# Kernel tuning notes

Hardware: AMD Instinct MI355X
Metric: run time of the kernel (lower is better)

## Reference

```python
import jax, jax.numpy as jnp
import numpy as np
from jax import lax

DG = 16          # deformable_groups
K = 9            # 3x3 kernel taps
PAD = 1
MAX_RES = 10.0   # max_residue_magnitude


def conv3x3(x, w, b):
    # NCHW / OIHW, stride 1, SAME padding (pad=1 for 3x3)
    return lax.conv_general_dilated(x, w, (1, 1), 'SAME',
                                    dimension_numbers=('NCHW', 'OIHW', 'NCHW')) + b[None, :, None, None]


def lrelu(x):
    return jnp.where(x >= 0, x, 0.1 * x)


def setup_inputs() -> dict:
    key = jax.random.key(0)
    ks = jax.random.split(key, 10)
    B, C, H, W = 4, 64, 128, 128
    Cout = 64
    coff_in = 2 * C + 2          # (1 + pa_frames//2)*C + pa_frames, pa_frames=2
    nch = 3 * K * DG             # 432 offset/mask channels

    def mkw(k, o, i, scale=1.0):
        return jax.random.normal(k, (o, i, 3, 3), jnp.float32) * (scale / np.sqrt(i * 9))

    return {
        'x': jax.random.normal(ks[0], (B, C, H, W), jnp.float32),
        'x_flow_warped': jax.random.normal(ks[1], (B, C, H, W), jnp.float32),
        'x_current': jax.random.normal(ks[2], (B, C, H, W), jnp.float32),
        'flow': jax.random.normal(ks[3], (B, 2, H, W), jnp.float32) * 2.0,
        'w1': mkw(ks[4], Cout, coff_in), 'b1': jnp.zeros((Cout,), jnp.float32),
        'w2': mkw(ks[5], Cout, Cout),    'b2': jnp.zeros((Cout,), jnp.float32),
        'w3': mkw(ks[6], Cout, Cout),    'b3': jnp.zeros((Cout,), jnp.float32),
        'w4': mkw(ks[7], nch, Cout, 0.1), 'b4': jnp.zeros((nch,), jnp.float32),
        'weight': mkw(ks[8], Cout, C),   'bias': jnp.zeros((Cout,), jnp.float32),
    }


def deform_conv2d(x, offset, mask, weight, bias):
    # modulated deformable conv, 3x3, stride 1, pad 1, dilation 1, groups=1
    B, C, H, W = x.shape
    O = weight.shape[0]
    dg, Cg = DG, C // DG
    off = offset.reshape(B, dg, K, 2, H, W)
    dy, dx = off[:, :, :, 0], off[:, :, :, 1]        # (B,dg,K,H,W), (y,x) pairs
    ki = jnp.arange(3)
    ii, jj = jnp.meshgrid(ki, ki, indexing='ij')
    ii = ii.reshape(K).astype(jnp.float32)
    jj = jj.reshape(K).astype(jnp.float32)
    # sampling coords in input space: h - pad + i + dy, w - pad + j + dx
    py = dy + (jnp.arange(H, dtype=jnp.float32) - PAD)[None, None, None, :, None] + ii[None, None, :, None, None]
    px = dx + (jnp.arange(W, dtype=jnp.float32) - PAD)[None, None, None, None, :] + jj[None, None, :, None, None]
    y0 = jnp.floor(py)
    x0 = jnp.floor(px)
    wy1 = py - y0
    wx1 = px - x0
    y0i = y0.astype(jnp.int32)
    x0i = x0.astype(jnp.int32)
    xg = x.reshape(B, dg, Cg, H * W)

    def gather(yi, xi):
        valid = ((yi >= 0) & (yi < H) & (xi >= 0) & (xi < W)).astype(x.dtype)  # zero outside
        idx = (jnp.clip(yi, 0, H - 1) * W + jnp.clip(xi, 0, W - 1)).reshape(B, dg, 1, K * H * W)
        v = jnp.take_along_axis(xg, jnp.broadcast_to(idx, (B, dg, Cg, K * H * W)), axis=-1)
        return v.reshape(B, dg, Cg, K, H, W) * valid[:, :, None]

    s = (gather(y0i, x0i)         * ((1 - wy1) * (1 - wx1))[:, :, None]
         + gather(y0i, x0i + 1)   * ((1 - wy1) * wx1)[:, :, None]
         + gather(y0i + 1, x0i)   * (wy1 * (1 - wx1))[:, :, None]
         + gather(y0i + 1, x0i + 1) * (wy1 * wx1)[:, :, None])
    s = s * mask.reshape(B, dg, 1, K, H, W)
    s = s.reshape(B, C, K, H, W)
    return jnp.einsum('bckhw,ock->bohw', s, weight.reshape(O, C, K)) + bias[None, :, None, None]


def reference(x, x_flow_warped, x_current, flow, w1, b1, w2, b2, w3, b3, w4, b4, weight, bias):
    feat = jnp.concatenate([x_flow_warped, x_current, flow], axis=1)
    h = lrelu(conv3x3(feat, w1, b1))
    h = lrelu(conv3x3(h, w2, b2))
    h = lrelu(conv3x3(h, w3, b3))
    out = conv3x3(h, w4, b4)
    o1, o2, mask = jnp.split(out, 3, axis=1)
    offset = MAX_RES * jnp.tanh(jnp.concatenate([o1, o2], axis=1))
    flowf = flow[:, ::-1]  # flip (x,y) -> (y,x)
    offset = offset + jnp.tile(flowf, (1, offset.shape[1] // 2, 1, 1))
    mask = jax.nn.sigmoid(mask)
    return deform_conv2d(x, offset, mask, weight, bias)
```

## Files before the change

### kernel.cpp

```cpp
#include <hip/hip_runtime.h>
#include <math.h>
#include <type_traits>

#define BH 4
#define HH 128
#define WW 128
#define HW (HH * WW)
#define SSTR 600

typedef __attribute__((ext_vector_type(8))) short bf16x8;
typedef __attribute__((ext_vector_type(4))) float f32x4;

__device__ inline short f2bf(float f) {
    union { float f; unsigned u; } x; x.f = f;
    unsigned r = x.u + 0x7fff + ((x.u >> 16) & 1);
    return (short)(r >> 16);
}
__device__ inline float bf2f(short h) {
    union { unsigned u; float f; } x; x.u = ((unsigned)(unsigned short)h) << 16;
    return x.f;
}
__device__ inline float bflo(unsigned u) {
    union { unsigned u; float f; } x; x.u = u << 16; return x.f;
}
__device__ inline float bfhi(unsigned u) {
    union { unsigned u; float f; } x; x.u = u & 0xffff0000u; return x.f;
}

struct RepackArgs {
    const float* w[5];
    short* dst[5];
    int off[6];
};

__device__ inline void repack_generic(const float* w, short* dst, int g,
                                      int M, int Cin, int T, int MT)
{
    int lane = g & 63;
    int f = g >> 6;
    int mt = f % MT;
    int kt = f / MT;
    int tap = kt % T;
    int kc = kt / T;
    int m = mt * 16 + (lane & 15);
    int ic0 = kc * 32 + (lane >> 4) * 8;
    short v[8];
#pragma unroll
    for (int i = 0; i < 8; ++i) {
        int ic = ic0 + i;
        float x = (m < M && ic < Cin) ? w[((size_t)m * Cin + ic) * T + tap] : 0.f;
        v[i] = f2bf(x);
    }
    *(bf16x8*)(dst + (size_t)g * 8) = *(const bf16x8*)v;
}

__global__ __launch_bounds__(256) void repack_all_k(RepackArgs a)
{
    int g = blockIdx.x * 256 + threadIdx.x;
    if (g < a.off[1]) {
        repack_generic(a.w[0], a.dst[0], g - a.off[0], 64, 130, 9, 4);
    } else if (g < a.off[2]) {
        repack_generic(a.w[1], a.dst[1], g - a.off[1], 64, 64, 9, 4);
    } else if (g < a.off[3]) {
        repack_generic(a.w[2], a.dst[2], g - a.off[2], 64, 64, 9, 4);
    } else if (g < a.off[4]) {
        repack_generic(a.w[3], a.dst[3], g - a.off[3], 432, 64, 9, 27);
    } else if (g < a.off[5]) {
        int gg = g - a.off[4];
        int lane = gg & 63;
        int f = gg >> 6;
        int mt = f & 3, kc = f >> 2;
        int m = mt * 16 + (lane & 15);
        int ck0 = kc * 32 + (lane >> 4) * 8;
        short v[8];
#pragma unroll
        for (int i = 0; i < 8; ++i) {
            int ck = ck0 + i;
            int dg = ck / 36, rem = ck % 36;
            int k = rem >> 2, cg = rem & 3;
            int c = dg * 4 + cg;
            v[i] = f2bf(a.w[4][((size_t)m * 64 + c) * 9 + k]);
        }
        *(bf16x8*)(a.dst[4] + (size_t)gg * 8) = *(const bf16x8*)v;
    }
}

__global__ __launch_bounds__(256) void prep_k(
    const float* __restrict__ xfw, const float* __restrict__ xcur,
    const float* __restrict__ flow, const float* __restrict__ x,
    short* __restrict__ cc, short* __restrict__ xt)
{
    int tid = threadIdx.x;
    int z = blockIdx.z;
    int px = blockIdx.x * 256 + tid;
    if (z < BH) {
        int b = z;
        const float* s0 = xfw + (size_t)b * 64 * HW + px;
        const float* s1 = xcur + (size_t)b * 64 * HW + px;
        const float* s2 = flow + (size_t)b * 2 * HW + px;
        short v[144];
#pragma unroll
        for (int c = 0; c < 64; ++c) v[c] = f2bf(s0[(size_t)c * HW]);
#pragma unroll
        for (int c = 0; c < 64; ++c) v[64 + c] = f2bf(s1[(size_t)c * HW]);
        v[128] = f2bf(s2[0]);
        v[129] = f2bf(s2[HW]);
#pragma unroll
        for (int c = 130; c < 144; ++c) v[c] = 0;
        short* dst = cc + ((size_t)b * HW + px) * 144;
#pragma unroll
        for (int q = 0; q < 18; ++q)
            *(bf16x8*)(dst + q * 8) = *(const bf16x8*)&v[q * 8];
    } else {
        int b = z - BH;
        const float* src = x + (size_t)b * 64 * HW + px;
        short v[64];
#pragma unroll
        for (int c = 0; c < 64; ++c) v[c] = f2bf(src[(size_t)c * HW]);
        short* dstb = xt + (size_t)b * 16 * HW * 4 + (size_t)px * 4;
#pragma unroll
        for (int d = 0; d < 16; ++d)
            *(uint2*)(dstb + (size_t)d * HW * 4) = *(const uint2*)&v[d * 4];
    }
}

template<int CSTR, int KC, bool ACT, int MTW>
__global__ __launch_bounds__(256) void conv_mfma_k(
    const short* __restrict__ in, const short* __restrict__ wp,
    const float* __restrict__ bias, short* __restrict__ out,
    int Cout, int MB, int MT)
{
    __shared__ alignas(16) short X[3 * 66 * 40];
    const int tid = threadIdx.x;
    const int lane = tid & 63, wv = tid >> 6;
    const int x0 = blockIdx.x * 64, y = blockIdx.y;
    const int zb = blockIdx.z;
    const int b = zb / MB, mb = zb % MB;

    int mtg[MTW];
#pragma unroll
    for (int mt = 0; mt < MTW; ++mt) {
        int t = (mb * 4 + wv) * MTW + mt;
        mtg[mt] = (t < MT) ? t : MT - 1;
    }

    const int r = tid / 66, c = tid - r * 66;
    const int yy = y + r - 1, xx = x0 + c - 1;
    const bool inb = (tid < 198) && (yy >= 0 && yy < HH && xx >= 0 && xx < WW);
    const short* srcp = in + ((size_t)b * HW + (size_t)yy * WW + xx) * CSTR;
    short* dstp = &X[(r * 66 + c) * 40];

    f32x4 acc[MTW][4] = {};

    for (int kc = 0; kc < KC; ++kc) {
        __syncthreads();
        if (tid < 198) {
            if (inb) {
                const short* s0 = srcp + kc * 32;
#pragma unroll
                for (int g = 0; g < 4; ++g)
                    *(bf16x8*)&dstp[g * 8] = *(const bf16x8*)&s0[g * 8];
            } else {
                bf16x8 z = {};
#pragma unroll
                for (int g = 0; g < 4; ++g) *(bf16x8*)&dstp[g * 8] = z;
            }
        }
        __syncthreads();
#pragma unroll
        for (int tap = 0; tap < 9; ++tap) {
            const int dy = tap / 3, dx = tap - dy * 3;
            bf16x8 a[MTW];
#pragma unroll
            for (int mt = 0; mt < MTW; ++mt)
                a[mt] = *(const bf16x8*)(wp + (((size_t)(kc * 9 + tap) * MT + mtg[mt]) * 64 + lane) * 8);
#pragma unroll
            for (int nt = 0; nt < 4; ++nt) {
                int cc2 = nt * 16 + (lane & 15) + dx;
                bf16x8 bb = *(const bf16x8*)&X[(dy * 66 + cc2) * 40 + (lane >> 4) * 8];
#pragma unroll
                for (int mt = 0; mt < MTW; ++mt)
                    acc[mt][nt] = __builtin_amdgcn_mfma_f32_16x16x32_bf16(a[mt], bb, acc[mt][nt], 0, 0, 0);
            }
        }
    }

    const int xl = lane & 15, rg = lane >> 4;
#pragma unroll
    for (int mt = 0; mt < MTW; ++mt) {
        int t = (mb * 4 + wv) * MTW + mt;
        int m0 = t * 16;
        if (m0 >= Cout) continue;
#pragma unroll
        for (int nt = 0; nt < 4; ++nt) {
            int xx2 = x0 + nt * 16 + xl;
            short pk[4];
#pragma unroll
            for (int j = 0; j < 4; ++j) {
                int o = m0 + rg * 4 + j;
                float rv = acc[mt][nt][j] + bias[o];
                if (ACT) rv = (rv >= 0.f) ? rv : 0.1f * rv;
                pk[j] = f2bf(rv);
            }
            *(uint2*)(out + ((size_t)b * HW + (size_t)y * WW + xx2) * (size_t)Cout
                      + m0 + rg * 4) = *(const uint2*)pk;
        }
    }
}

__global__ __launch_bounds__(256) void dcn_k(
    const short* __restrict__ xt, const float* __restrict__ flow,
    const short* __restrict__ out4, const short* __restrict__ wtp,
    const float* __restrict__ bias, float* __restrict__ out)
{
    __shared__ alignas(16) short s[16 * SSTR];
    const int tid = threadIdx.x;
    const int b = blockIdx.z, y = blockIdx.y, xb = blockIdx.x * 16;
    const size_t hw = (size_t)HW;
    constexpr float L2E = 1.4426950408889634f;

    const int lane = tid & 63, wv = tid >> 6;
    const int p = tid & 15;
    const int dg = tid >> 4;
    const int xp = xb + p;
    const size_t pix = (size_t)y * WW + xp;
    const short* xg = xt + ((size_t)b * 16 + dg) * hw * 4;
    const short* o4p = out4 + ((size_t)b * hw + pix) * 432;
    const float fl0 = flow[((size_t)b * 2 + 0) * hw + pix];
    const float fl1 = flow[((size_t)b * 2 + 1) * hw + pix];

    const unsigned* pd = (const unsigned*)o4p + 9 * dg;
    const short* pm = o4p + 288 + 9 * dg;
    short* sp = &s[p * SSTR + dg * 36];

#pragma unroll
    for (int it = 0; it < 9; ++it) {
        unsigned dyx = pd[it];
        float omk = bf2f(pm[it]);
        float ody = bflo(dyx), odx = bfhi(dyx);
        float tdy = 1.f - 2.f * __builtin_amdgcn_rcpf(__builtin_amdgcn_exp2f(2.f * L2E * ody) + 1.f);
        float tdx = 1.f - 2.f * __builtin_amdgcn_rcpf(__builtin_amdgcn_exp2f(2.f * L2E * odx) + 1.f);
        float m   = __builtin_amdgcn_rcpf(1.f + __builtin_amdgcn_exp2f(-L2E * omk));

        float py = 10.f * tdy + fl1 + (float)(y  - 1 + it / 3);
        float px = 10.f * tdx + fl0 + (float)(xp - 1 + it % 3);
        float fy = floorf(py), fx = floorf(px);
        int iy0 = (int)fy, ix0 = (int)fx;
        float wy1 = py - fy, wx1 = px - fx;
        float wy0 = 1.f - wy1, wx0 = 1.f - wx1;
        int iy1 = iy0 + 1, ix1 = ix0 + 1;
        bool vy0 = (iy0 >= 0) & (iy0 < HH), vy1 = (iy1 >= 0) & (iy1 < HH);
        bool vx0 = (ix0 >= 0) & (ix0 < WW), vx1 = (ix1 >= 0) & (ix1 < WW);
        float w00 = (vy0 & vx0) ? wy0 * wx0 : 0.f;
        float w01 = (vy0 & vx1) ? wy0 * wx1 : 0.f;
        float w10 = (vy1 & vx0) ? wy1 * wx0 : 0.f;
        float w11 = (vy1 & vx1) ? wy1 * wx1 : 0.f;
        int cy0 = min(max(iy0, 0), HH - 1), cy1 = min(max(iy1, 0), HH - 1);
        int cx0 = min(max(ix0, 0), WW - 1), cx1 = min(max(ix1, 0), WW - 1);
        uint2 d00 = *(const uint2*)(xg + (size_t)(cy0 * WW + cx0) * 4);
        uint2 d01 = *(const uint2*)(xg + (size_t)(cy0 * WW + cx1) * 4);
        uint2 d10 = *(const uint2*)(xg + (size_t)(cy1 * WW + cx0) * 4);
        uint2 d11 = *(const uint2*)(xg + (size_t)(cy1 * WW + cx1) * 4);

        float a0 = w00 * bflo(d00.x) + w01 * bflo(d01.x) + w10 * bflo(d10.x) + w11 * bflo(d11.x);
        float a1 = w00 * bfhi(d00.x) + w01 * bfhi(d01.x) + w10 * bfhi(d10.x) + w11 * bfhi(d11.x);
        float a2 = w00 * bflo(d00.y) + w01 * bflo(d01.y) + w10 * bflo(d10.y) + w11 * bflo(d11.y);
        float a3 = w00 * bfhi(d00.y) + w01 * bfhi(d01.y) + w10 * bfhi(d10.y) + w11 * bfhi(d11.y);

        uint2 t;
        t.x = ((unsigned)(unsigned short)f2bf(a1 * m) << 16) | (unsigned short)f2bf(a0 * m);
        t.y = ((unsigned)(unsigned short)f2bf(a3 * m) << 16) | (unsigned short)f2bf(a2 * m);
        *(uint2*)&sp[it * 4] = t;
    }
    __syncthreads();

    f32x4 acc = {};
#pragma unroll
    for (int kc = 0; kc < 18; ++kc) {
        bf16x8 a = *(const bf16x8*)(wtp + ((size_t)(kc * 4 + wv) * 64 + lane) * 8);
        bf16x8 bb = *(const bf16x8*)&s[(lane & 15) * SSTR + kc * 32 + (lane >> 4) * 8];
        acc = __builtin_amdgcn_mfma_f32_16x16x32_bf16(a, bb, acc, 0, 0, 0);
    }

    const int xl = lane & 15, rg = lane >> 4;
#pragma unroll
    for (int j = 0; j < 4; ++j) {
        int o = wv * 16 + rg * 4 + j;
        out[((size_t)(b * 64 + o) * HH + y) * WW + xb + xl] = acc[j] + bias[o];
    }
}

extern "C" void kernel_launch(void* const* d_in, const int* in_sizes, int n_in,
                              void* d_out, int out_size, void* d_ws, size_t ws_size,
                              hipStream_t stream)
{
    const float* x    = (const float*)d_in[0];
    const float* xfw  = (const float*)d_in[1];
    const float* xcur = (const float*)d_in[2];
    const float* flow = (const float*)d_in[3];
    const float* w1   = (const float*)d_in[4];
    const float* b1   = (const float*)d_in[5];
    const float* w2   = (const float*)d_in[6];
    const float* b2   = (const float*)d_in[7];
    const float* w3   = (const float*)d_in[8];
    const float* b3   = (const float*)d_in[9];
    const float* w4   = (const float*)d_in[10];
    const float* b4   = (const float*)d_in[11];
    const float* wt   = (const float*)d_in[12];
    const float* bs   = (const float*)d_in[13];

    const size_t hw = (size_t)HW;
    short* out4 = (short*)d_ws;
    short* h1   = out4 + (size_t)BH * hw * 432;
    short* h2   = h1 + (size_t)BH * hw * 64;
    short* cc   = h2 + (size_t)BH * hw * 64;
    short* xt   = cc + (size_t)BH * hw * 144 + 256;
    short* wp1  = xt + (size_t)BH * hw * 64 + 256;
    short* wp2  = wp1 + (size_t)180 * 512;
    short* wp3  = wp2 + (size_t)72 * 512;
    short* wp4  = wp3 + (size_t)72 * 512;
    short* wtp  = wp4 + (size_t)486 * 512;

    RepackArgs ra;
    ra.w[0] = w1; ra.w[1] = w2; ra.w[2] = w3; ra.w[3] = w4; ra.w[4] = wt;
    ra.dst[0] = wp1; ra.dst[1] = wp2; ra.dst[2] = wp3; ra.dst[3] = wp4; ra.dst[4] = wtp;
    int tot[5] = {11520, 4608, 4608, 31104, 4608};
    ra.off[0] = 0;
    for (int i = 0; i < 5; ++i) ra.off[i + 1] = ra.off[i] + tot[i];
    repack_all_k<<<(ra.off[5] + 255) / 256, 256, 0, stream>>>(ra);

    prep_k<<<dim3(HW / 256, 1, 2 * BH), 256, 0, stream>>>(xfw, xcur, flow, x, cc, xt);

    dim3 blk(256);
    conv_mfma_k<144, 5, true,  1><<<dim3(2, 128, BH),      blk, 0, stream>>>(cc, wp1, b1, h1, 64, 1, 4);
    conv_mfma_k<64,  2, true,  1><<<dim3(2, 128, BH),      blk, 0, stream>>>(h1, wp2, b2, h2, 64, 1, 4);
    conv_mfma_k<64,  2, true,  1><<<dim3(2, 128, BH),      blk, 0, stream>>>(h2, wp3, b3, h1, 64, 1, 4);
    conv_mfma_k<64,  2, false, 4><<<dim3(2, 128, BH * 2),  blk, 0, stream>>>(h1, wp4, b4, out4, 432, 2, 27);

    dcn_k<<<dim3(WW / 16, HH, BH), blk, 0, stream>>>(xt, flow, out4, wtp, bs, (float*)d_out);
}
```

Baseline: 205.3 us.

## Fuse tanh/sigmoid/flow offset epilogue into conv4 and register-prefetch conv input chunks

Moves the tanh, scale-by-10, flow addition and sigmoid mask activation from the deformable conv kernel into the epilogue of the last offset conv, so out4 now stores final offsets and masks and dcn_k drops its flow loads and transcendental work. Separately, the conv kernel now loads the next input channel chunk into registers while the MFMA loop runs on the current chunk, overlapping global loads with compute. Storing final offsets in bf16 instead of pre-activation values changes rounding: an offset of magnitude around 100 keeps less fractional precision, which can affect bilinear sampling accuracy.

New measurement: 236.8 us. 1.15x slower.

```diff
diff --git a/kernel.cpp b/kernel.cpp
--- a/kernel.cpp
+++ b/kernel.cpp
@@ -124,11 +124,11 @@
     }
 }
 
-template<int CSTR, int KC, bool ACT, int MTW>
+template<int CSTR, int KC, bool ACT, int MTW, bool DCNT>
 __global__ __launch_bounds__(256) void conv_mfma_k(
     const short* __restrict__ in, const short* __restrict__ wp,
-    const float* __restrict__ bias, short* __restrict__ out,
-    int Cout, int MB, int MT)
+    const float* __restrict__ bias, const float* __restrict__ flow,
+    short* __restrict__ out, int Cout, int MB, int MT)
 {
     __shared__ alignas(16) short X[3 * 66 * 40];
     const int tid = threadIdx.x;
@@ -136,6 +136,7 @@
     const int x0 = blockIdx.x * 64, y = blockIdx.y;
     const int zb = blockIdx.z;
     const int b = zb / MB, mb = zb % MB;
+    constexpr float L2E = 1.4426950408889634f;
 
     int mtg[MTW];
 #pragma unroll
@@ -146,27 +147,37 @@
 
     const int r = tid / 66, c = tid - r * 66;
     const int yy = y + r - 1, xx = x0 + c - 1;
-    const bool inb = (tid < 198) && (yy >= 0 && yy < HH && xx >= 0 && xx < WW);
+    const bool stg_act = (tid < 198);
+    const bool inb = stg_act && (yy >= 0 && yy < HH && xx >= 0 && xx < WW);
     const short* srcp = in + ((size_t)b * HW + (size_t)yy * WW + xx) * CSTR;
     short* dstp = &X[(r * 66 + c) * 40];
 
+    bf16x8 stg0 = {}, stg1 = {}, stg2 = {}, stg3 = {};
+    if (inb) {
+        stg0 = *(const bf16x8*)&srcp[0];
+        stg1 = *(const bf16x8*)&srcp[8];
+        stg2 = *(const bf16x8*)&srcp[16];
+        stg3 = *(const bf16x8*)&srcp[24];
+    }
+
     f32x4 acc[MTW][4] = {};
 
     for (int kc = 0; kc < KC; ++kc) {
         __syncthreads();
-        if (tid < 198) {
-            if (inb) {
-                const short* s0 = srcp + kc * 32;
-#pragma unroll
-                for (int g = 0; g < 4; ++g)
-                    *(bf16x8*)&dstp[g * 8] = *(const bf16x8*)&s0[g * 8];
-            } else {
-                bf16x8 z = {};
-#pragma unroll
-                for (int g = 0; g < 4; ++g) *(bf16x8*)&dstp[g * 8] = z;
-            }
+        if (stg_act) {
+            *(bf16x8*)&dstp[0]  = stg0;
+            *(bf16x8*)&dstp[8]  = stg1;
+            *(bf16x8*)&dstp[16] = stg2;
+            *(bf16x8*)&dstp[24] = stg3;
         }
         __syncthreads();
+        if (inb && kc + 1 < KC) {
+            const short* s0 = srcp + (kc + 1) * 32;
+            stg0 = *(const bf16x8*)&s0[0];
+            stg1 = *(const bf16x8*)&s0[8];
+            stg2 = *(const bf16x8*)&s0[16];
+            stg3 = *(const bf16x8*)&s0[24];
+        }
 #pragma unroll
         for (int tap = 0; tap < 9; ++tap) {
             const int dy = tap / 3, dx = tap - dy * 3;
@@ -187,19 +198,34 @@
 
     const int xl = lane & 15, rg = lane >> 4;
 #pragma unroll
-    for (int mt = 0; mt < MTW; ++mt) {
-        int t = (mb * 4 + wv) * MTW + mt;
-        int m0 = t * 16;
-        if (m0 >= Cout) continue;
-#pragma unroll
-        for (int nt = 0; nt < 4; ++nt) {
-            int xx2 = x0 + nt * 16 + xl;
+    for (int nt = 0; nt < 4; ++nt) {
+        int xx2 = x0 + nt * 16 + xl;
+        float fl0 = 0.f, fl1 = 0.f;
+        if (DCNT) {
+            size_t pix = (size_t)y * WW + xx2;
+            fl0 = flow[((size_t)b * 2 + 0) * HW + pix];
+            fl1 = flow[((size_t)b * 2 + 1) * HW + pix];
+        }
+#pragma unroll
+        for (int mt = 0; mt < MTW; ++mt) {
+            int t = (mb * 4 + wv) * MTW + mt;
+            int m0 = t * 16;
+            if (m0 >= Cout) continue;
             short pk[4];
 #pragma unroll
             for (int j = 0; j < 4; ++j) {
                 int o = m0 + rg * 4 + j;
                 float rv = acc[mt][nt][j] + bias[o];
                 if (ACT) rv = (rv >= 0.f) ? rv : 0.1f * rv;
+                if (DCNT) {
+                    if (o < 288) {
+                        float th = 1.f - 2.f * __builtin_amdgcn_rcpf(
+                            __builtin_amdgcn_exp2f(2.f * L2E * rv) + 1.f);
+                        rv = 10.f * th + ((o & 1) ? fl0 : fl1);
+                    } else {
+                        rv = __builtin_amdgcn_rcpf(1.f + __builtin_amdgcn_exp2f(-L2E * rv));
+                    }
+                }
                 pk[j] = f2bf(rv);
             }
             *(uint2*)(out + ((size_t)b * HW + (size_t)y * WW + xx2) * (size_t)Cout
@@ -209,15 +235,14 @@
 }
 
 __global__ __launch_bounds__(256) void dcn_k(
-    const short* __restrict__ xt, const float* __restrict__ flow,
-    const short* __restrict__ out4, const short* __restrict__ wtp,
-    const float* __restrict__ bias, float* __restrict__ out)
+    const short* __restrict__ xt, const short* __restrict__ out4,
+    const short* __restrict__ wtp, const float* __restrict__ bias,
+    float* __restrict__ out)
 {
     __shared__ alignas(16) short s[16 * SSTR];
     const int tid = threadIdx.x;
     const int b = blockIdx.z, y = blockIdx.y, xb = blockIdx.x * 16;
     const size_t hw = (size_t)HW;
-    constexpr float L2E = 1.4426950408889634f;
 
     const int lane = tid & 63, wv = tid >> 6;
     const int p = tid & 15;
@@ -226,8 +251,6 @@
     const size_t pix = (size_t)y * WW + xp;
     const short* xg = xt + ((size_t)b * 16 + dg) * hw * 4;
     const short* o4p = out4 + ((size_t)b * hw + pix) * 432;
-    const float fl0 = flow[((size_t)b * 2 + 0) * hw + pix];
-    const float fl1 = flow[((size_t)b * 2 + 1) * hw + pix];
 
     const unsigned* pd = (const unsigned*)o4p + 9 * dg;
     const short* pm = o4p + 288 + 9 * dg;
@@ -236,14 +259,11 @@
 #pragma unroll
     for (int it = 0; it < 9; ++it) {
         unsigned dyx = pd[it];
-        float omk = bf2f(pm[it]);
-        float ody = bflo(dyx), odx = bfhi(dyx);
-        float tdy = 1.f - 2.f * __builtin_amdgcn_rcpf(__builtin_amdgcn_exp2f(2.f * L2E * ody) + 1.f);
-        float tdx = 1.f - 2.f * __builtin_amdgcn_rcpf(__builtin_amdgcn_exp2f(2.f * L2E * odx) + 1.f);
-        float m   = __builtin_amdgcn_rcpf(1.f + __builtin_amdgcn_exp2f(-L2E * omk));
-
-        float py = 10.f * tdy + fl1 + (float)(y  - 1 + it / 3);
-        float px = 10.f * tdx + fl0 + (float)(xp - 1 + it % 3);
+        float m = bf2f(pm[it]);
+        float dyf = bflo(dyx), dxf = bfhi(dyx);
+
+        float py = dyf + (float)(y  - 1 + it / 3);
+        float px = dxf + (float)(xp - 1 + it % 3);
         float fy = floorf(py), fx = floorf(px);
         int iy0 = (int)fy, ix0 = (int)fx;
         float wy1 = py - fy, wx1 = px - fx;
@@ -332,10 +352,10 @@
     prep_k<<<dim3(HW / 256, 1, 2 * BH), 256, 0, stream>>>(xfw, xcur, flow, x, cc, xt);
 
     dim3 blk(256);
-    conv_mfma_k<144, 5, true,  1><<<dim3(2, 128, BH),      blk, 0, stream>>>(cc, wp1, b1, h1, 64, 1, 4);
-    conv_mfma_k<64,  2, true,  1><<<dim3(2, 128, BH),      blk, 0, stream>>>(h1, wp2, b2, h2, 64, 1, 4);
-    conv_mfma_k<64,  2, true,  1><<<dim3(2, 128, BH),      blk, 0, stream>>>(h2, wp3, b3, h1, 64, 1, 4);
-    conv_mfma_k<64,  2, false, 4><<<dim3(2, 128, BH * 2),  blk, 0, stream>>>(h1, wp4, b4, out4, 432, 2, 27);
-
-    dcn_k<<<dim3(WW / 16, HH, BH), blk, 0, stream>>>(xt, flow, out4, wtp, bs, (float*)d_out);
-}
+    conv_mfma_k<144, 5, true,  1, false><<<dim3(2, 128, BH),     blk, 0, stream>>>(cc, wp1, b1, nullptr, h1, 64, 1, 4);
+    conv_mfma_k<64,  2, true,  1, false><<<dim3(2, 128, BH),     blk, 0, stream>>>(h1, wp2, b2, nullptr, h2, 64, 1, 4);
+    conv_mfma_k<64,  2, true,  1, false><<<dim3(2, 128, BH),     blk, 0, stream>>>(h2, wp3, b3, nullptr, h1, 64, 1, 4);
+    conv_mfma_k<64,  2, false, 4, true ><<<dim3(2, 128, BH * 2), blk, 0, stream>>>(h1, wp4, b4, flow, out4, 432, 2, 27);
+
+    dcn_k<<<dim3(WW / 16, HH, BH), blk, 0, stream>>>(xt, out4, wtp, bs, (float*)d_out);
+}
```
